# Kernel tuning notes

Hardware: AMD Instinct MI355X
Metric: run time of the kernel (lower is better)

The kernel has to match this reference:

```python
import jax, jax.numpy as jnp
import numpy as np

B, M = 2, 8192          # clouds per batch, points per cloud (N = B*M)
K_NEAR, K_FAR, K_SMOOTH = 8, 16, 8
T_LOC, T_CON = 0.1, 0.5
EPS = 1e-8


def setup_inputs() -> dict:
    key = jax.random.key(0)
    k1, k2 = jax.random.split(key)
    scores = jax.random.uniform(k1, (B * M,), dtype=jnp.float32)          # in [0,1]
    coords = jax.random.normal(k2, (B * M, 3), dtype=jnp.float32) * 2.0   # point positions
    batch_ids = (jnp.arange(B * M, dtype=jnp.int32) // M).astype(jnp.int32)
    return {"scores": scores, "coords": coords, "batch_ids": batch_ids}


def _knn_global(coords):
    """Per-cloud brute-force kNN (self included as first neighbor, like pointops.knn_query).
    coords: (N,3) -> global indices (N, K_FAR)."""
    c = coords.reshape(B, M, 3)

    def per_cloud(cb):  # cb: (M,3)
        sq = jnp.sum(cb * cb, axis=-1)                      # (M,)
        d2 = sq[:, None] + sq[None, :] - 2.0 * (cb @ cb.T)  # (M,M) squared dists
        _, idx = jax.lax.top_k(-d2, K_FAR)                  # (M,K_FAR) smallest dists
        return idx

    idx = jax.vmap(per_cloud)(c)                            # (B,M,K_FAR) local indices
    idx = idx + (jnp.arange(B, dtype=idx.dtype) * M)[:, None, None]
    return idx.reshape(B * M, K_FAR)


def _loss_terms(scores, coords, idx):
    # --- locality: neighbors (incl. self) should have similar scores ---
    nb = idx[:, :K_NEAR]                                    # (N,k)
    score_diff = jnp.abs(scores[:, None] - scores[nb])      # (N,k)
    dists = jnp.linalg.norm(coords[:, None, :] - coords[nb], axis=2)  # (N,k)
    w = jnp.exp(-dists / T_LOC)
    loss_loc = jnp.sum(w * score_diff ** 2) / jnp.clip(jnp.sum(w), 1e-8)

    # --- contrastive: near similar, far dissimilar ---
    sim_pos = 1.0 - jnp.abs(scores[:, None] - scores[idx[:, :K_NEAR]])
    sim_neg = 1.0 - jnp.abs(scores[:, None] - scores[idx[:, K_NEAR:K_FAR]])
    loss_pos = -jnp.mean(jnp.log(jax.nn.sigmoid(sim_pos / T_CON) + EPS))
    loss_neg = -jnp.mean(jnp.log(1.0 - jax.nn.sigmoid(sim_neg / T_CON) + EPS))
    loss_con = loss_pos + loss_neg

    # --- distribution: sorted scores match uniform linspace per cloud ---
    sb = jnp.sort(scores.reshape(B, M), axis=1)             # (B,M)
    target = jnp.linspace(0.0, 1.0, M, dtype=scores.dtype)  # (M,)
    loss_dist = jnp.mean(jnp.mean((sb - target[None, :]) ** 2, axis=1))

    # --- smoothness: score close to neighbor mean ---
    nmean = jnp.mean(scores[idx[:, :K_SMOOTH]], axis=1)     # (N,)
    loss_smooth = jnp.mean((scores - nmean) ** 2)

    return loss_loc, loss_con, loss_dist, loss_smooth


def reference(scores, coords, batch_ids):
    del batch_ids  # equal-sized clouds; batch structure is (B, M) by construction
    idx = _knn_global(coords)
    l_loc, l_con, l_dist, l_smooth = _loss_terms(scores, coords, idx)
    total = 1.0 * l_loc + 0.5 * l_con + 0.3 * l_dist + 0.2 * l_smooth
    return total
```

## Files before the change

kernel.cpp:

```cpp
#include <hip/hip_runtime.h>
#include <hip/hip_bf16.h>
#include <math.h>

#define BB 2
#define MM 8192
#define NN (BB * MM)
#define NBATCH (NN / 16)
#define NCELL 4096
#define LOSS_BLOCKS 1024

#define PART_OFF   0
#define RANK_OFF   24576
#define IDX_OFF    90112
#define PK_OFF     1138688
#define SS_OFF     1400832
#define CELLID_OFF 1466368
#define CNT_OFF    1531904
#define CUR_OFF    1564672
#define BBLO_OFF   1597440
#define BBHI_OFF   1613824
#define PKEY_OFF   1630208

__device__ __forceinline__ unsigned mort3(unsigned x, unsigned y, unsigned z) {
    unsigned m = 0;
#pragma unroll
    for (int i = 0; i < 4; ++i) {
        m |= ((x >> i) & 1u) << (3 * i);
        m |= ((y >> i) & 1u) << (3 * i + 1);
        m |= ((z >> i) & 1u) << (3 * i + 2);
    }
    return m;
}

__global__ void count_kernel(const float* __restrict__ coords, int* __restrict__ cellid,
                             int* __restrict__ cnt) {
    int i = blockIdx.x * 256 + threadIdx.x;
    if (i < NN) {
        float x = coords[3 * i], y = coords[3 * i + 1], z = coords[3 * i + 2];
        int cx = min(15, max(0, (int)floorf(x) + 8));
        int cy = min(15, max(0, (int)floorf(y) + 8));
        int cz = min(15, max(0, (int)floorf(z) + 8));
        int cid = (i >> 13) * NCELL + (int)mort3((unsigned)cx, (unsigned)cy, (unsigned)cz);
        cellid[i] = cid;
        atomicAdd(&cnt[cid], 1);
    }
}

__global__ __launch_bounds__(1024) void scan_kernel(const int* __restrict__ cnt,
                                                    int* __restrict__ cursor) {
    __shared__ int wsum[16];
    const int tid = threadIdx.x, lane = tid & 63, wv = tid >> 6;
    int v[8]; int run = 0;
#pragma unroll
    for (int i = 0; i < 8; ++i) { int t = cnt[tid * 8 + i]; v[i] = run; run += t; }
    int inc = run;
#pragma unroll
    for (int off = 1; off < 64; off <<= 1) {
        int y = __shfl_up(inc, off);
        if (lane >= off) inc += y;
    }
    int laneExcl = inc - run;
    if (lane == 63) wsum[wv] = inc;
    __syncthreads();
    int wbase = 0;
#pragma unroll
    for (int w = 0; w < 16; ++w) wbase += (w < wv) ? wsum[w] : 0;
    const int base = wbase + laneExcl;
#pragma unroll
    for (int i = 0; i < 8; ++i) cursor[tid * 8 + i] = base + v[i];
}

__global__ void scatter_kernel(const float* __restrict__ coords, const float* __restrict__ scores,
                               const int* __restrict__ cellid, int* __restrict__ cursor,
                               float4* __restrict__ pk_s, float* __restrict__ s_s) {
    int i = blockIdx.x * 256 + threadIdx.x;
    if (i < NN) {
        int pos = atomicAdd(&cursor[cellid[i]], 1);
        float x = coords[3 * i], y = coords[3 * i + 1], z = coords[3 * i + 2];
        float sq = fmaf(x, x, fmaf(y, y, z * z));
        pk_s[pos] = make_float4(x, y, z, sq);
        s_s[pos] = scores[i];
    }
}

__global__ void bbox_kernel(const float4* __restrict__ pk_s, float4* __restrict__ bb_lo,
                            float4* __restrict__ bb_hi) {
    int b = blockIdx.x * 256 + threadIdx.x;
    if (b < NBATCH) {
        float4 c = pk_s[b * 16];
        float lx = c.x, ly = c.y, lz = c.z, hx = c.x, hy = c.y, hz = c.z;
#pragma unroll
        for (int i = 1; i < 16; ++i) {
            c = pk_s[b * 16 + i];
            lx = fminf(lx, c.x); ly = fminf(ly, c.y); lz = fminf(lz, c.z);
            hx = fmaxf(hx, c.x); hy = fmaxf(hy, c.y); hz = fmaxf(hz, c.z);
        }
        bb_lo[b] = make_float4(lx, ly, lz, 0.f);
        bb_hi[b] = make_float4(hx, hy, hz, 0.f);
    }
}

__device__ __forceinline__ void sort16(unsigned (&a)[16]) {
#pragma unroll
    for (int p2 = 1; p2 < 16; p2 <<= 1) {
#pragma unroll
        for (int k2 = p2; k2 >= 1; k2 >>= 1) {
#pragma unroll
            for (int j2 = k2 % p2; j2 + k2 < 16; j2 += 2 * k2) {
#pragma unroll
                for (int i2 = 0; i2 < k2; ++i2) {
                    if (i2 + j2 + k2 < 16) {
                        if (((i2 + j2) / (2 * p2)) == ((i2 + j2 + k2) / (2 * p2))) {
                            unsigned x = a[i2 + j2], y = a[i2 + j2 + k2];
                            a[i2 + j2]      = min(x, y);
                            a[i2 + j2 + k2] = max(x, y);
                        }
                    }
                }
            }
        }
    }
}

__device__ __forceinline__ void truncmerge(unsigned (&slot)[16], const unsigned (&kb)[16]) {
    unsigned m[16];
#pragma unroll
    for (int k = 0; k < 16; ++k) m[k] = min(slot[k], kb[15 - k]);
#pragma unroll
    for (int st = 8; st >= 1; st >>= 1) {
#pragma unroll
        for (int i = 0; i < 16; ++i) {
            if ((i & st) == 0) {
                unsigned lo = min(m[i], m[i + st]);
                unsigned hi = max(m[i], m[i + st]);
                m[i] = lo; m[i + st] = hi;
            }
        }
    }
#pragma unroll
    for (int k = 0; k < 16; ++k) slot[k] = m[k];
}

__global__ __launch_bounds__(1024) void knn_kernel(const float4* __restrict__ pk_s,
                                                   const float4* __restrict__ bb_lo,
                                                   const float4* __restrict__ bb_hi,
                                                   unsigned* __restrict__ pkeys) {
    __shared__ unsigned lds_k[16][16][64];
    __shared__ unsigned lds_tmin[64];
    const int tid = threadIdx.x, lane = tid & 63;
    const int wv = __builtin_amdgcn_readfirstlane(tid >> 6);
    const int g  = blockIdx.x >> 2;
    const int qt = blockIdx.x & 3;
    const int qbase = g << 6;
    const int cloudbase = (qbase >> 13) << 13;
    const float4 p = pk_s[qbase + lane];
    const int sb0 = (qbase - cloudbase) >> 4;
    const float4* __restrict__ pc = pk_s + cloudbase;
    const int bbase = cloudbase >> 4;
    const int qt0 = qt << 7;

    if (tid < 64) lds_tmin[tid] = 0x7f7fffffu;

    unsigned slot[16];
#pragma unroll
    for (int k = 0; k < 16; ++k) slot[k] = 0x7F000000u + (unsigned)k;

    auto loadkeys = [&](int bi, unsigned (&kb)[16]) {
#pragma unroll
        for (int i = 0; i < 16; ++i) {
            const int j = bi * 16 + i;
            const float4 c = pc[j];
            float dot = fmaf(p.x, c.x, fmaf(p.y, c.y, p.z * c.z));
            float d2  = fmaf(-2.0f, dot, p.w + c.w);
            kb[i] = (__float_as_uint(d2) & 0xFFFFE000u) | (unsigned)j;
        }
    };

    auto batch = [&](int bi, float tbound) {
        unsigned kb[16];
        loadkeys(bi, kb);
        unsigned kmin = kb[0];
#pragma unroll
        for (int i = 1; i < 16; ++i) kmin = min(kmin, kb[i]);
        const bool useful = (kmin < slot[15]) &&
                            (__uint_as_float(kmin & 0xFFFFE000u) < tbound);
        if (__any(useful)) {
            sort16(kb);
            truncmerge(slot, kb);
            atomicMin(&lds_tmin[lane], (slot[15] & 0xFFFFE000u) + 0x2000u);
        }
    };

    const int r = sb0 & 15;
    const int ownb = (wv >= r && wv < r + 4) ? (sb0 + (wv - r)) : -1;
    __syncthreads();
    if (ownb >= 0) {
        unsigned kb[16];
        loadkeys(ownb, kb);
        sort16(kb);
        atomicMin(&lds_tmin[lane], (kb[15] & 0xFFFFE000u) + 0x2000u);
    }
    __syncthreads();

    float4 lo = bb_lo[bbase + qt0 + wv];
    float4 hi = bb_hi[bbase + qt0 + wv];
    for (int k = 0; k < 8; ++k) {
        const int bi = qt0 + wv + (k << 4);
        float4 lo_n, hi_n;
        if (k + 1 < 8) {
            lo_n = bb_lo[bbase + bi + 16];
            hi_n = bb_hi[bbase + bi + 16];
        }
        const bool isSeed = (bi >= sb0 && bi < sb0 + 4);
        if (!isSeed) {
            const float tsh = __uint_as_float(lds_tmin[lane]);
            float dx = fmaxf(fmaxf(lo.x - p.x, p.x - hi.x), 0.f);
            float dy = fmaxf(fmaxf(lo.y - p.y, p.y - hi.y), 0.f);
            float dz = fmaxf(fmaxf(lo.z - p.z, p.z - hi.z), 0.f);
            float lb = fmaf(dx, dx, fmaf(dy, dy, dz * dz));
            if (__any(fmaf(lb, 0.999f, -1e-5f) < tsh)) batch(bi, tsh);
        } else {
            const float tsh = __uint_as_float(lds_tmin[lane]);
            batch(bi, tsh);
        }
        lo = lo_n; hi = hi_n;
    }

#pragma unroll
    for (int k = 0; k < 16; ++k) lds_k[wv][k][lane] = slot[k];

    for (int half = 8; half >= 1; half >>= 1) {
        __syncthreads();
        if (wv < half) {
            unsigned a[16], m[16];
#pragma unroll
            for (int k = 0; k < 16; ++k) a[k] = lds_k[wv][k][lane];
#pragma unroll
            for (int k = 0; k < 16; ++k) m[k] = min(a[k], lds_k[wv + half][15 - k][lane]);
#pragma unroll
            for (int st = 8; st >= 1; st >>= 1) {
#pragma unroll
                for (int i = 0; i < 16; ++i) {
                    if ((i & st) == 0) {
                        unsigned lo2 = min(m[i], m[i + st]);
                        unsigned hi2 = max(m[i], m[i + st]);
                        m[i] = lo2; m[i + st] = hi2;
                    }
                }
            }
#pragma unroll
            for (int k = 0; k < 16; ++k) lds_k[wv][k][lane] = m[k];
        }
    }
    __syncthreads();

    if (wv == 0) {
#pragma unroll
        for (int k = 0; k < 16; ++k)
            pkeys[(unsigned)(blockIdx.x * 16 + k) * 64 + lane] = lds_k[0][k][lane];
    }
}

__global__ __launch_bounds__(256) void merge4_kernel(const unsigned* __restrict__ pkeys,
                                                     int* __restrict__ out_idx) {
    const int t = blockIdx.x * 256 + threadIdx.x;
    const int g = t >> 6, lane = t & 63;
    const int cloudbase = (g >> 7) << 13;
    unsigned a[16];
#pragma unroll
    for (int k = 0; k < 16; ++k) a[k] = pkeys[(unsigned)((g * 4 + 0) * 16 + k) * 64 + lane];
#pragma unroll
    for (int qt = 1; qt < 4; ++qt) {
        unsigned b[16];
#pragma unroll
        for (int k = 0; k < 16; ++k) b[k] = pkeys[(unsigned)((g * 4 + qt) * 16 + k) * 64 + lane];
        truncmerge(a, b);
    }
#pragma unroll
    for (int k = 0; k < 16; ++k)
        out_idx[(g * 64 + lane) * 16 + k] = (int)(a[k] & 0x1FFFu) + cloudbase;
}

__global__ __launch_bounds__(1024) void rank_kernel(const float* __restrict__ s_s,
                                                    int* __restrict__ out_rank) {
    __shared__ int lds_r[16][64];
    const int tid = threadIdx.x, lane = tid & 63;
    const int wv = __builtin_amdgcn_readfirstlane(tid >> 6);
    const int qbase = blockIdx.x * 64;
    const int cloudbase = (qbase >> 13) << 13;
    const float s = s_s[qbase + lane];
    const float* __restrict__ sc = s_s + cloudbase;
    int rank = 0;
    const int j0 = wv * 512;
    for (int jj = 0; jj < 512; jj += 16) {
#pragma unroll
        for (int i = 0; i < 16; ++i) {
            rank += (sc[j0 + jj + i] < s) ? 1 : 0;
        }
    }
    lds_r[wv][lane] = rank;
    __syncthreads();
    if (wv == 0) {
        int rsum = 0;
#pragma unroll
        for (int w = 0; w < 16; ++w) rsum += lds_r[w][lane];
        out_rank[qbase + lane] = rsum;
    }
}

__global__ __launch_bounds__(256) void loss_kernel(const float* __restrict__ s_s,
                                                   const float4* __restrict__ pk_s,
                                                   const int* __restrict__ knn,
                                                   const int* __restrict__ rank,
                                                   float* __restrict__ partial) {
    __shared__ float red[4][6];
    const int t = blockIdx.x * 256 + threadIdx.x;
    const int q = t >> 4, k = t & 15;
    const int nb = knn[t];
    const float s  = s_s[q];
    const float sn = s_s[nb];
    const float diff = fabsf(s - sn);
    const float sim = 1.0f - diff;
    const float sg = 1.0f / (1.0f + expf(-2.0f * sim));

    float a_wd = 0.f, a_w = 0.f, a_pos = 0.f, a_neg = 0.f, snk = 0.f;
    if (k < 8) {
        float4 pq = pk_s[q];
        float4 pn = pk_s[nb];
        float dx = pq.x - pn.x, dy = pq.y - pn.y, dz = pq.z - pn.z;
        float d = sqrtf(dx * dx + dy * dy + dz * dz);
        float w = expf(-10.0f * d);
        a_wd = w * diff * diff;
        a_w  = w;
        a_pos = logf(sg + 1e-8f);
        snk = sn;
    } else {
        a_neg = logf(1.0f - sg + 1e-8f);
    }

    float nsum = snk;
#pragma unroll
    for (int off = 1; off < 16; off <<= 1) nsum += __shfl_xor(nsum, off);

    float a_sm = 0.f, a_di = 0.f;
    if (k == 0) {
        float t1 = s - nsum * 0.125f;
        a_sm = t1 * t1;
        float t2 = s - (float)rank[q] * (1.0f / 8191.0f);
        a_di = t2 * t2;
    }

#pragma unroll
    for (int off = 1; off < 64; off <<= 1) {
        a_wd  += __shfl_xor(a_wd, off);
        a_w   += __shfl_xor(a_w, off);
        a_pos += __shfl_xor(a_pos, off);
        a_neg += __shfl_xor(a_neg, off);
        a_sm  += __shfl_xor(a_sm, off);
        a_di  += __shfl_xor(a_di, off);
    }
    const int wv = threadIdx.x >> 6;
    if ((threadIdx.x & 63) == 0) {
        red[wv][0] = a_wd; red[wv][1] = a_w; red[wv][2] = a_pos;
        red[wv][3] = a_neg; red[wv][4] = a_sm; red[wv][5] = a_di;
    }
    __syncthreads();
    if (threadIdx.x < 6) {
        float v = red[0][threadIdx.x] + red[1][threadIdx.x] +
                  red[2][threadIdx.x] + red[3][threadIdx.x];
        partial[threadIdx.x * LOSS_BLOCKS + blockIdx.x] = v;
    }
}

__global__ __launch_bounds__(1024) void fin_kernel(const float* __restrict__ partial,
                                                   float* __restrict__ out) {
    __shared__ float red[16][6];
    const int tid = threadIdx.x;
    float a[6];
#pragma unroll
    for (int term = 0; term < 6; ++term) a[term] = partial[term * LOSS_BLOCKS + tid];
#pragma unroll
    for (int off = 1; off < 64; off <<= 1) {
#pragma unroll
        for (int term = 0; term < 6; ++term) a[term] += __shfl_xor(a[term], off);
    }
    if ((tid & 63) == 0) {
#pragma unroll
        for (int term = 0; term < 6; ++term) red[tid >> 6][term] = a[term];
    }
    __syncthreads();
    if (tid == 0) {
        float acc[6];
#pragma unroll
        for (int term = 0; term < 6; ++term) {
            float v = 0.f;
#pragma unroll
            for (int w = 0; w < 16; ++w) v += red[w][term];
            acc[term] = v;
        }
        float l_loc = acc[0] / fmaxf(acc[1], 1e-8f);
        float l_pos = -acc[2] / (float)(NN * 8);
        float l_neg = -acc[3] / (float)(NN * 8);
        float l_sm  = acc[4] / (float)NN;
        float l_di  = acc[5] / (float)NN;
        out[0] = l_loc + 0.5f * (l_pos + l_neg) + 0.3f * l_di + 0.2f * l_sm;
    }
}

extern "C" void kernel_launch(void* const* d_in, const int* in_sizes, int n_in,
                              void* d_out, int out_size, void* d_ws, size_t ws_size,
                              hipStream_t stream) {
    const float* scores = (const float*)d_in[0];
    const float* coords = (const float*)d_in[1];
    (void)in_sizes; (void)n_in; (void)out_size; (void)ws_size;

    char* ws = (char*)d_ws;
    float*  part  = (float*)(ws + PART_OFF);
    int*    rank  = (int*)(ws + RANK_OFF);
    int*    knn   = (int*)(ws + IDX_OFF);
    float4* pk_s  = (float4*)(ws + PK_OFF);
    float*  s_s   = (float*)(ws + SS_OFF);
    int*    cellid= (int*)(ws + CELLID_OFF);
    int*    cnt   = (int*)(ws + CNT_OFF);
    int*    cursor= (int*)(ws + CUR_OFF);
    float4* bb_lo = (float4*)(ws + BBLO_OFF);
    float4* bb_hi = (float4*)(ws + BBHI_OFF);
    unsigned* pkeys = (unsigned*)(ws + PKEY_OFF);
    float*  out   = (float*)d_out;

    hipMemsetAsync(cnt, 0, 2 * NCELL * sizeof(int), stream);
    count_kernel<<<64, 256, 0, stream>>>(coords, cellid, cnt);
    scan_kernel<<<1, 1024, 0, stream>>>(cnt, cursor);
    scatter_kernel<<<64, 256, 0, stream>>>(coords, scores, cellid, cursor, pk_s, s_s);
    bbox_kernel<<<4, 256, 0, stream>>>(pk_s, bb_lo, bb_hi);
    knn_kernel<<<1024, 1024, 0, stream>>>(pk_s, bb_lo, bb_hi, pkeys);
    merge4_kernel<<<64, 256, 0, stream>>>(pkeys, knn);
    rank_kernel<<<256, 1024, 0, stream>>>(s_s, rank);
    loss_kernel<<<LOSS_BLOCKS, 256, 0, stream>>>(s_s, pk_s, knn, rank, part);
    fin_kernel<<<1, 1024, 0, stream>>>(part, out);
}
```

Before: 158.1 us.

## Halve kNN block waves and replace sort-merge with per-candidate skip insertion

The kNN kernel now runs 8 waves per block instead of 16, so each wave scans 16 candidate batches rather than 8. The sort16-plus-truncmerge step is replaced by a per-key insertion into the sorted slot list, skipped when no lane's key beats the current 16th-best. Seed batches in the query's own tile are inserted directly instead of only setting the threshold. The aim is less sorting work for the many candidates that fail pruning and a shorter LDS reduction tree, at the cost of fewer waves per block and a longer serial loop in each wave.

```diff
diff --git a/kernel.cpp b/kernel.cpp
--- a/kernel.cpp
+++ b/kernel.cpp
@@ -141,11 +141,11 @@
     for (int k = 0; k < 16; ++k) slot[k] = m[k];
 }
 
-__global__ __launch_bounds__(1024) void knn_kernel(const float4* __restrict__ pk_s,
-                                                   const float4* __restrict__ bb_lo,
-                                                   const float4* __restrict__ bb_hi,
-                                                   unsigned* __restrict__ pkeys) {
-    __shared__ unsigned lds_k[16][16][64];
+__global__ __launch_bounds__(512) void knn_kernel(const float4* __restrict__ pk_s,
+                                                  const float4* __restrict__ bb_lo,
+                                                  const float4* __restrict__ bb_hi,
+                                                  unsigned* __restrict__ pkeys) {
+    __shared__ unsigned lds_k[8][16][64];
     __shared__ unsigned lds_tmin[64];
     const int tid = threadIdx.x, lane = tid & 63;
     const int wv = __builtin_amdgcn_readfirstlane(tid >> 6);
@@ -158,6 +158,7 @@
     const float4* __restrict__ pc = pk_s + cloudbase;
     const int bbase = cloudbase >> 4;
     const int qt0 = qt << 7;
+    const int qs  = sb0 >> 7;
 
     if (tid < 64) lds_tmin[tid] = 0x7f7fffffu;
 
@@ -176,52 +177,63 @@
         }
     };
 
-    auto batch = [&](int bi, float tbound) {
+    auto batchIns = [&](int bi, float tb) {
         unsigned kb[16];
         loadkeys(bi, kb);
         unsigned kmin = kb[0];
 #pragma unroll
         for (int i = 1; i < 16; ++i) kmin = min(kmin, kb[i]);
         const bool useful = (kmin < slot[15]) &&
-                            (__uint_as_float(kmin & 0xFFFFE000u) < tbound);
-        if (__any(useful)) {
+                            (__uint_as_float(kmin & 0xFFFFE000u) < tb);
+        if (!__any(useful)) return;
+        bool ins = false;
+#pragma unroll
+        for (int i = 0; i < 16; ++i) {
+            if (__any(kb[i] < slot[15])) {
+                unsigned c = kb[i];
+#pragma unroll
+                for (int k = 0; k < 16; ++k) {
+                    unsigned lo = min(slot[k], c);
+                    c = max(slot[k], c);
+                    slot[k] = lo;
+                }
+                ins = true;
+            }
+        }
+        if (ins) atomicMin(&lds_tmin[lane], (slot[15] & 0xFFFFE000u) + 0x2000u);
+    };
+
+    const int d = (wv - (sb0 & 7)) & 7;
+    const int seedb = (d < 4) ? sb0 + d : -1;
+    __syncthreads();
+    if (seedb >= 0) {
+        if (qt == qs) {
+            batchIns(seedb, 3.0e38f);
+        } else {
+            unsigned kb[16];
+            loadkeys(seedb, kb);
             sort16(kb);
-            truncmerge(slot, kb);
-            atomicMin(&lds_tmin[lane], (slot[15] & 0xFFFFE000u) + 0x2000u);
-        }
-    };
-
-    const int r = sb0 & 15;
-    const int ownb = (wv >= r && wv < r + 4) ? (sb0 + (wv - r)) : -1;
-    __syncthreads();
-    if (ownb >= 0) {
-        unsigned kb[16];
-        loadkeys(ownb, kb);
-        sort16(kb);
-        atomicMin(&lds_tmin[lane], (kb[15] & 0xFFFFE000u) + 0x2000u);
+            atomicMin(&lds_tmin[lane], (kb[15] & 0xFFFFE000u) + 0x2000u);
+        }
     }
     __syncthreads();
 
     float4 lo = bb_lo[bbase + qt0 + wv];
     float4 hi = bb_hi[bbase + qt0 + wv];
-    for (int k = 0; k < 8; ++k) {
-        const int bi = qt0 + wv + (k << 4);
+    for (int k = 0; k < 16; ++k) {
+        const int bi = qt0 + wv + (k << 3);
         float4 lo_n, hi_n;
-        if (k + 1 < 8) {
-            lo_n = bb_lo[bbase + bi + 16];
-            hi_n = bb_hi[bbase + bi + 16];
-        }
-        const bool isSeed = (bi >= sb0 && bi < sb0 + 4);
-        if (!isSeed) {
+        if (k + 1 < 16) {
+            lo_n = bb_lo[bbase + bi + 8];
+            hi_n = bb_hi[bbase + bi + 8];
+        }
+        if (bi != seedb || qt != qs) {
             const float tsh = __uint_as_float(lds_tmin[lane]);
             float dx = fmaxf(fmaxf(lo.x - p.x, p.x - hi.x), 0.f);
             float dy = fmaxf(fmaxf(lo.y - p.y, p.y - hi.y), 0.f);
             float dz = fmaxf(fmaxf(lo.z - p.z, p.z - hi.z), 0.f);
             float lb = fmaf(dx, dx, fmaf(dy, dy, dz * dz));
-            if (__any(fmaf(lb, 0.999f, -1e-5f) < tsh)) batch(bi, tsh);
-        } else {
-            const float tsh = __uint_as_float(lds_tmin[lane]);
-            batch(bi, tsh);
+            if (__any(fmaf(lb, 0.999f, -1e-5f) < tsh)) batchIns(bi, tsh);
         }
         lo = lo_n; hi = hi_n;
     }
@@ -229,7 +241,7 @@
 #pragma unroll
     for (int k = 0; k < 16; ++k) lds_k[wv][k][lane] = slot[k];
 
-    for (int half = 8; half >= 1; half >>= 1) {
+    for (int half = 4; half >= 1; half >>= 1) {
         __syncthreads();
         if (wv < half) {
             unsigned a[16], m[16];
@@ -433,7 +445,7 @@
     scan_kernel<<<1, 1024, 0, stream>>>(cnt, cursor);
     scatter_kernel<<<64, 256, 0, stream>>>(coords, scores, cellid, cursor, pk_s, s_s);
     bbox_kernel<<<4, 256, 0, stream>>>(pk_s, bb_lo, bb_hi);
-    knn_kernel<<<1024, 1024, 0, stream>>>(pk_s, bb_lo, bb_hi, pkeys);
+    knn_kernel<<<1024, 512, 0, stream>>>(pk_s, bb_lo, bb_hi, pkeys);
     merge4_kernel<<<64, 256, 0, stream>>>(pkeys, knn);
     rank_kernel<<<256, 1024, 0, stream>>>(s_s, rank);
     loss_kernel<<<LOSS_BLOCKS, 256, 0, stream>>>(s_s, pk_s, knn, rank, part);
```

Result: slower. 185.0 us (+17.0%).
